# Optimization experiments

Hardware: AMD Instinct MI355X
Metric: run time of the kernel (lower is better)

## Reference

```python
import jax, jax.numpy as jnp
import numpy as np

# Multi-scale feature pyramid (H, W) per level, as produced by a DETR backbone
SPATIAL_SHAPES = [(100, 100), (50, 50), (25, 25), (13, 13)]
LEVEL_START = np.cumsum([0] + [h * w for h, w in SPATIAL_SHAPES])[:-1]
LEN = sum(h * w for h, w in SPATIAL_SHAPES)  # 13294
B = 2
D = 256      # d_model
NH = 8       # n_heads
NL = 4       # n_levels
NP = 4       # n_points
DH = D // NH
DFF = 1024
EPS = 1e-5


def setup_inputs() -> dict:
    key = jax.random.key(0)
    ks = jax.random.split(key, 16)
    w = lambda k, sh: jax.random.normal(k, sh, jnp.float32) * 0.02
    return {
        'src': jax.random.normal(ks[0], (B, LEN, D), jnp.float32),
        'pos': jax.random.normal(ks[1], (B, LEN, D), jnp.float32) * 0.02,
        'reference_points': jax.random.uniform(ks[2], (B, LEN, NL, 2), jnp.float32),
        'W_value': w(ks[3], (D, D)), 'b_value': jnp.zeros((D,), jnp.float32),
        'W_off': w(ks[4], (D, NH * NL * NP * 2)), 'b_off': w(ks[5], (NH * NL * NP * 2,)),
        'W_attn': w(ks[6], (D, NH * NL * NP)), 'b_attn': jnp.zeros((NH * NL * NP,), jnp.float32),
        'W_out': w(ks[7], (D, D)), 'b_out': jnp.zeros((D,), jnp.float32),
        'W1': w(ks[8], (D, DFF)), 'b1': jnp.zeros((DFF,), jnp.float32),
        'W2': w(ks[9], (DFF, D)), 'b2': jnp.zeros((D,), jnp.float32),
        'g1': jnp.ones((D,), jnp.float32), 'be1': jnp.zeros((D,), jnp.float32),
        'g2': jnp.ones((D,), jnp.float32), 'be2': jnp.zeros((D,), jnp.float32),
    }


def layer_norm(x, g, b):
    m = jnp.mean(x, -1, keepdims=True)
    v = jnp.mean((x - m) ** 2, -1, keepdims=True)
    return (x - m) * jax.lax.rsqrt(v + EPS) * g + b


def ms_deform_attn(query, src, ref, W_value, b_value, W_off, b_off, W_attn, b_attn, W_out, b_out):
    Bq, L, _ = query.shape
    value = (src @ W_value + b_value).reshape(Bq, L, NH, DH)
    off = (query @ W_off + b_off).reshape(Bq, L, NH, NL, NP, 2)
    attw = jax.nn.softmax((query @ W_attn + b_attn).reshape(Bq, L, NH, NL * NP), axis=-1)
    attw = attw.reshape(Bq, L, NH, NL, NP)
    # normalizer is (W, H) per level, matching offset_normalizer in MSDeformAttn
    wh = jnp.array([[w_, h_] for h_, w_ in SPATIAL_SHAPES], jnp.float32)
    loc = ref[:, :, None, :, None, :] + off / wh[None, None, None, :, None, :]  # (B,L,NH,NL,NP,2)

    out = jnp.zeros((Bq, L, NH, DH), value.dtype)
    for l, (H, W) in enumerate(SPATIAL_SHAPES):
        s = int(LEVEL_START[l])
        vl = value[:, s:s + H * W]  # (B, H*W, NH, DH)
        # grid_sample(align_corners=False): pixel = loc * size - 0.5
        x = loc[:, :, :, l, :, 0] * W - 0.5  # (B, L, NH, NP)
        y = loc[:, :, :, l, :, 1] * H - 0.5
        x = jnp.transpose(x, (0, 1, 3, 2)).reshape(Bq, L * NP, NH)
        y = jnp.transpose(y, (0, 1, 3, 2)).reshape(Bq, L * NP, NH)
        x0 = jnp.floor(x); y0 = jnp.floor(y)
        dx = x - x0; dy = y - y0
        x0i = x0.astype(jnp.int32); y0i = y0.astype(jnp.int32)
        acc = jnp.zeros((Bq, L * NP, NH, DH), value.dtype)
        corners = [
            (x0i,     y0i,     (1 - dx) * (1 - dy)),
            (x0i + 1, y0i,     dx * (1 - dy)),
            (x0i,     y0i + 1, (1 - dx) * dy),
            (x0i + 1, y0i + 1, dx * dy),
        ]
        for xi, yi, wgt in corners:
            inb = (xi >= 0) & (xi < W) & (yi >= 0) & (yi < H)  # zero padding
            idx = jnp.clip(yi, 0, H - 1) * W + jnp.clip(xi, 0, W - 1)
            g = jnp.take_along_axis(vl, idx[..., None], axis=1)  # (B, L*NP, NH, DH)
            acc = acc + g * (wgt * inb)[..., None]
        acc = acc.reshape(Bq, L, NP, NH, DH)
        w_l = jnp.transpose(attw[:, :, :, l, :], (0, 1, 3, 2))  # (B, L, NP, NH)
        out = out + jnp.sum(acc * w_l[..., None], axis=2)
    return out.reshape(Bq, L, D) @ W_out + b_out


def reference(src, pos, reference_points,
              W_value, b_value, W_off, b_off, W_attn, b_attn, W_out, b_out,
              W1, b1, W2, b2, g1, be1, g2, be2):
    # DeformableTransformerEncoderLayer.forward (dropout = identity at eval)
    query = src + pos
    src2 = ms_deform_attn(query, src, reference_points,
                          W_value, b_value, W_off, b_off, W_attn, b_attn, W_out, b_out)
    src = layer_norm(src + src2, g1, be1)
    ffn = jax.nn.relu(src @ W1 + b1) @ W2 + b2
    src = layer_norm(src + ffn, g2, be2)
    return src
```

## Files before the change

kernel.cpp:

```cpp
#include <hip/hip_runtime.h>
#include <hip/hip_bf16.h>

#define LENQ 13294
#define MROWS 26588
#define PADM  26624
#define EPS_LN 1e-5f

typedef __attribute__((ext_vector_type(8))) short short8;
typedef __attribute__((ext_vector_type(4))) float vf4;

__device__ inline ushort f2bf(float f) {
    __hip_bfloat16 h = __float2bfloat16(f);
    return reinterpret_cast<ushort&>(h);
}
__device__ inline float bfbits2f(uint lo16) {
    return __uint_as_float(lo16 << 16);
}

__device__ inline void load_lds16(const void* g, void* l) {
    __builtin_amdgcn_global_load_lds(
        (const __attribute__((address_space(1))) unsigned int*)g,
        (__attribute__((address_space(3))) unsigned int*)l,
        16, 0, 0);
}

__global__ __launch_bounds__(256) void wconv_all(
    const float* __restrict__ Wv, const float* __restrict__ Woff,
    const float* __restrict__ Wattn, const float* __restrict__ Wout,
    const float* __restrict__ W1, const float* __restrict__ W2,
    ushort* __restrict__ wvt, ushort* __restrict__ woat,
    ushort* __restrict__ woutt, ushort* __restrict__ w1t, ushort* __restrict__ w2t)
{
    const int bid = blockIdx.x;
    const float* src; ushort* dst; int K, N, tb;
    if      (bid < 64)  { src = Wv;    dst = wvt;            K = 256;  N = 256;  tb = bid; }
    else if (bid < 128) { src = Woff;  dst = woat;           K = 256;  N = 256;  tb = bid - 64; }
    else if (bid < 160) { src = Wattn; dst = woat + 256*256; K = 256;  N = 128;  tb = bid - 128; }
    else if (bid < 224) { src = Wout;  dst = woutt;          K = 256;  N = 256;  tb = bid - 160; }
    else if (bid < 480) { src = W1;    dst = w1t;            K = 256;  N = 1024; tb = bid - 224; }
    else                { src = W2;    dst = w2t;            K = 1024; N = 256;  tb = bid - 480; }
    const int ntn = N >> 5;
    const int kt = tb / ntn, nt = tb % ntn;

    __shared__ float s[32][36];
    const int t = threadIdx.x;
    const int ty = t >> 3, tx = (t & 7) * 4;
    float4 v = *reinterpret_cast<const float4*>(src + (size_t)(kt*32 + ty) * N + nt*32 + tx);
    s[ty][tx+0] = v.x; s[ty][tx+1] = v.y; s[ty][tx+2] = v.z; s[ty][tx+3] = v.w;
    __syncthreads();
    ushort4 o;
    o.x = f2bf(s[tx+0][ty]); o.y = f2bf(s[tx+1][ty]);
    o.z = f2bf(s[tx+2][ty]); o.w = f2bf(s[tx+3][ty]);
    *reinterpret_cast<ushort4*>(dst + (size_t)(nt*32 + ty) * K + kt*32 + tx) = o;
}

__global__ __launch_bounds__(256) void conv_src_q(
    const float* __restrict__ src, const float* __restrict__ pos,
    ushort* __restrict__ srcb, ushort* __restrict__ qb)
{
    const int i = blockIdx.x * 256 + threadIdx.x;
    const int row = i >> 6;
    const int c4 = i & 63;
    const int sr = min(row, MROWS - 1);
    float4 s = reinterpret_cast<const float4*>(src)[(size_t)sr * 64 + c4];
    float4 p = reinterpret_cast<const float4*>(pos)[(size_t)sr * 64 + c4];
    ushort4 sb, qv;
    sb.x = f2bf(s.x); sb.y = f2bf(s.y); sb.z = f2bf(s.z); sb.w = f2bf(s.w);
    qv.x = f2bf(s.x + p.x); qv.y = f2bf(s.y + p.y);
    qv.z = f2bf(s.z + p.z); qv.w = f2bf(s.w + p.w);
    reinterpret_cast<ushort4*>(srcb)[(size_t)row * 64 + c4] = sb;
    reinterpret_cast<ushort4*>(qb)[(size_t)row * 64 + c4]   = qv;
}

template<int MF, bool RELU>
__global__ __launch_bounds__(256) void gemm_lds(
    const ushort* __restrict__ A, const ushort* __restrict__ Bt,
    const float* __restrict__ bias0, const float* __restrict__ bias1, int nsplit,
    ushort* __restrict__ C, int N, int K)
{
    constexpr int BM = MF * 32;
    __shared__ short As[BM * 32];
    __shared__ short Bs[128 * 32];

    const int t = threadIdx.x;
    const int m0 = blockIdx.x * BM, n0 = blockIdx.y * 128;
    const int lane = t & 63, w = t >> 6;
    const int wr = w >> 1, wc = w & 1;
    const int ln = lane & 15, lr = lane >> 4;
    const int swz = (lr ^ ((ln >> 1) & 3)) * 8;
    const int cg = (((lane & 3) ^ ((lane >> 3) & 3))) * 8;
    const int srow = lane >> 2;

    vf4 acc[MF][4];
    #pragma unroll
    for (int m = 0; m < MF; ++m)
        #pragma unroll
        for (int n = 0; n < 4; ++n)
            acc[m][n] = (vf4){0.f, 0.f, 0.f, 0.f};

    const int bch0 = 2 * w, bch1 = 2 * w + 1;
    const ushort* gB0 = Bt + (size_t)(n0 + bch0 * 16 + srow) * K + cg;
    const ushort* gB1 = Bt + (size_t)(n0 + bch1 * 16 + srow) * K + cg;
    short* lB0 = Bs + bch0 * 512;
    short* lB1 = Bs + bch1 * 512;
    const int ach0 = (MF == 4) ? 2 * w : w;
    const ushort* gA0 = A + (size_t)(m0 + ach0 * 16 + srow) * K + cg;
    short* lA0 = As + ach0 * 512;
    const ushort* gA1 = A + (size_t)(m0 + (2 * w + 1) * 16 + srow) * K + cg;
    short* lA1 = As + (2 * w + 1) * 512;

    for (int k0 = 0; k0 < K; k0 += 32) {
        __syncthreads();
        load_lds16(gA0 + k0, lA0);
        if constexpr (MF == 4) load_lds16(gA1 + k0, lA1);
        load_lds16(gB0 + k0, lB0);
        load_lds16(gB1 + k0, lB1);
        __syncthreads();

        short8 af[MF], bfr[4];
        #pragma unroll
        for (int m = 0; m < MF; ++m)
            af[m] = *reinterpret_cast<const short8*>(&As[(wr * (MF * 16) + m * 16 + ln) * 32 + swz]);
        #pragma unroll
        for (int n = 0; n < 4; ++n)
            bfr[n] = *reinterpret_cast<const short8*>(&Bs[(wc * 64 + n * 16 + ln) * 32 + swz]);
        #pragma unroll
        for (int m = 0; m < MF; ++m)
            #pragma unroll
            for (int n = 0; n < 4; ++n)
                acc[m][n] = __builtin_amdgcn_mfma_f32_16x16x32_bf16(af[m], bfr[n], acc[m][n], 0, 0, 0);
    }

    #pragma unroll
    for (int n = 0; n < 4; ++n) {
        const int col = n0 + wc * 64 + n * 16 + ln;
        const float b = (col < nsplit) ? bias0[col] : bias1[col - nsplit];
        #pragma unroll
        for (int m = 0; m < MF; ++m) {
            const int rbase = m0 + wr * (MF * 16) + m * 16 + lr * 4;
            #pragma unroll
            for (int q = 0; q < 4; ++q) {
                float v = acc[m][n][q] + b;
                if (RELU) v = fmaxf(v, 0.f);
                C[(size_t)(rbase + q) * N + col] = f2bf(v);
            }
        }
    }
}

__global__ __launch_bounds__(256) void ms_sample(
    const ushort* __restrict__ value, const ushort* __restrict__ oa,
    const float* __restrict__ ref, ushort* __restrict__ outb)
{
    __shared__ uint2 s_iw[32 * 68];

    const int t    = threadIdx.x;
    const int row0 = blockIdx.x * 4;

    #pragma unroll
    for (int j = 0; j < 2; ++j) {
        const int item = t + j * 256;
        const int r = item >> 7, h = (item >> 4) & 7, lp = item & 15;
        const int l = lp >> 2;
        const int row = row0 + r;
        const int bsel = (row >= LENQ) ? 1 : 0;

        const float lg = bfbits2f(oa[(size_t)row * 384 + 256 + h * 16 + lp]);
        float mx = lg;
        #pragma unroll
        for (int s2 = 1; s2 < 16; s2 <<= 1) mx = fmaxf(mx, __shfl_xor(mx, s2));
        const float e = __expf(lg - mx);
        float se = e;
        #pragma unroll
        for (int s2 = 1; s2 < 16; s2 <<= 1) se += __shfl_xor(se, s2);
        const float aw = e / se;

        const int W = (int)((0x0D193264u >> (l * 8)) & 0xffu);
        const int LS = (l == 0) ? 0 : (l == 1) ? 10000 : (l == 2) ? 12500 : 13125;
        const uint oxy = *reinterpret_cast<const uint*>(oa + (size_t)row * 384 + (h * 16 + lp) * 2);
        const float ox = bfbits2f(oxy & 0xffffu);
        const float oy = __uint_as_float(oxy & 0xffff0000u);
        const float rx = ref[(size_t)row * 8 + l * 2 + 0];
        const float ry = ref[(size_t)row * 8 + l * 2 + 1];
        const float fw = (float)W;
        const float x = (rx + ox / fw) * fw - 0.5f;
        const float y = (ry + oy / fw) * fw - 0.5f;
        const float fx = floorf(x), fy = floorf(y);
        const float dx = x - fx, dy = y - fy;
        const int x0 = (int)fx, y0 = (int)fy;
        const int gbase = bsel * LENQ + LS;
        uint2* dst = &s_iw[(r * 8 + h) * 68 + lp * 4];
        #pragma unroll
        for (int cy = 0; cy < 2; ++cy)
            #pragma unroll
            for (int cx = 0; cx < 2; ++cx) {
                const int xi = x0 + cx, yi = y0 + cy;
                const bool in = (xi >= 0) && (xi < W) && (yi >= 0) && (yi < W);
                const int xc = min(max(xi, 0), W - 1);
                const int yc = min(max(yi, 0), W - 1);
                const float wgt = in ? ((cx ? dx : 1.f - dx) * (cy ? dy : 1.f - dy) * aw) : 0.f;
                dst[cy * 2 + cx] = make_uint2((uint)((gbase + yc * W + xc) * 256),
                                              __float_as_uint(wgt));
            }
    }
    __syncthreads();

    const int r = t >> 6, h = (t >> 3) & 7, c4 = t & 7;
    const int row = row0 + r;
    const ushort* vb = value + h * 32 + c4 * 4;
    const uint2* iw = &s_iw[(r * 8 + h) * 68];
    float4 acc = make_float4(0.f, 0.f, 0.f, 0.f);
    #pragma unroll 8
    for (int e = 0; e < 64; ++e) {
        const uint2 w = iw[e];
        const float wt = __uint_as_float(w.y);
        const uint2 gv = *reinterpret_cast<const uint2*>(vb + w.x);
        acc.x += wt * __uint_as_float(gv.x << 16);
        acc.y += wt * __uint_as_float(gv.x & 0xffff0000u);
        acc.z += wt * __uint_as_float(gv.y << 16);
        acc.w += wt * __uint_as_float(gv.y & 0xffff0000u);
    }
    ushort4 o;
    o.x = f2bf(acc.x); o.y = f2bf(acc.y); o.z = f2bf(acc.z); o.w = f2bf(acc.w);
    *reinterpret_cast<ushort4*>(outb + (size_t)row * 256 + h * 32 + c4 * 4) = o;
}

template<bool AF32, bool WF32>
__global__ __launch_bounds__(256) void resid_ln(
    const float* __restrict__ af, const ushort* __restrict__ ab,
    const ushort* __restrict__ r,
    const float* __restrict__ g, const float* __restrict__ be,
    float* __restrict__ outf, ushort* __restrict__ outb, int M)
{
    const int lane = threadIdx.x & 63;
    const int wid  = threadIdx.x >> 6;
    const int row  = blockIdx.x * 4 + wid;
    if (row >= M) return;

    float4 va;
    if (AF32) {
        va = *(reinterpret_cast<const float4*>(af + (size_t)row * 256) + lane);
    } else {
        ushort4 ua = *(reinterpret_cast<const ushort4*>(ab + (size_t)row * 256) + lane);
        va.x = bfbits2f(ua.x); va.y = bfbits2f(ua.y);
        va.z = bfbits2f(ua.z); va.w = bfbits2f(ua.w);
    }
    ushort4 ur = *(reinterpret_cast<const ushort4*>(r + (size_t)row * 256) + lane);
    float4 v;
    v.x = va.x + bfbits2f(ur.x); v.y = va.y + bfbits2f(ur.y);
    v.z = va.z + bfbits2f(ur.z); v.w = va.w + bfbits2f(ur.w);

    float s = v.x + v.y + v.z + v.w;
    #pragma unroll
    for (int m = 1; m < 64; m <<= 1) s += __shfl_xor(s, m);
    const float mean = s * (1.f / 256.f);

    float4 d;
    d.x = v.x - mean; d.y = v.y - mean; d.z = v.z - mean; d.w = v.w - mean;
    float q = d.x * d.x + d.y * d.y + d.z * d.z + d.w * d.w;
    #pragma unroll
    for (int m = 1; m < 64; m <<= 1) q += __shfl_xor(q, m);
    const float rs = rsqrtf(q * (1.f / 256.f) + EPS_LN);

    float4 gv = *(reinterpret_cast<const float4*>(g) + lane);
    float4 bv = *(reinterpret_cast<const float4*>(be) + lane);
    float4 o;
    o.x = d.x * rs * gv.x + bv.x;
    o.y = d.y * rs * gv.y + bv.y;
    o.z = d.z * rs * gv.z + bv.z;
    o.w = d.w * rs * gv.w + bv.w;
    if (WF32) {
        *(reinterpret_cast<float4*>(outf + (size_t)row * 256) + lane) = o;
    } else {
        ushort4 h;
        h.x = f2bf(o.x); h.y = f2bf(o.y); h.z = f2bf(o.z); h.w = f2bf(o.w);
        *(reinterpret_cast<ushort4*>(outb + (size_t)row * 256) + lane) = h;
    }
}

extern "C" void kernel_launch(void* const* d_in, const int* in_sizes, int n_in,
                              void* d_out, int out_size, void* d_ws, size_t ws_size,
                              hipStream_t stream)
{
    const float* src   = (const float*)d_in[0];
    const float* pos   = (const float*)d_in[1];
    const float* refp  = (const float*)d_in[2];
    const float* Wv    = (const float*)d_in[3];
    const float* bv    = (const float*)d_in[4];
    const float* Woff  = (const float*)d_in[5];
    const float* boff  = (const float*)d_in[6];
    const float* Wattn = (const float*)d_in[7];
    const float* battn = (const float*)d_in[8];
    const float* Wout  = (const float*)d_in[9];
    const float* bout  = (const float*)d_in[10];
    const float* W1    = (const float*)d_in[11];
    const float* b1    = (const float*)d_in[12];
    const float* W2    = (const float*)d_in[13];
    const float* b2    = (const float*)d_in[14];
    const float* g1    = (const float*)d_in[15];
    const float* be1   = (const float*)d_in[16];
    const float* g2    = (const float*)d_in[17];
    const float* be2   = (const float*)d_in[18];
    float* out = (float*)d_out;

    char* wsb = (char*)d_ws;
    const size_t SB   = (size_t)PADM * 256 * 2;
    const size_t OABS = (size_t)PADM * 384 * 2;
    ushort* srcb   = (ushort*)(wsb);
    ushort* qb     = (ushort*)(wsb + SB);
    ushort* valueb = (ushort*)(wsb + 2 * SB);
    ushort* oab    = (ushort*)(wsb + 3 * SB);
    ushort* attnb  = (ushort*)(wsb + 3 * SB + OABS);
    ushort* src2b  = (ushort*)(wsb + 4 * SB + OABS);
    ushort* ffnb   = src2b;
    ushort* x1b    = (ushort*)(wsb + 5 * SB + OABS);
    ushort* hb     = (ushort*)(wsb);
    char*   wgt    = wsb + 6 * SB + OABS;
    ushort* wvt    = (ushort*)(wgt);
    ushort* woat   = (ushort*)(wgt + 131072);
    ushort* woutt  = (ushort*)(wgt + 327680);
    ushort* w1t    = (ushort*)(wgt + 458752);
    ushort* w2t    = (ushort*)(wgt + 983040);

    const dim3 blk(256);

    wconv_all<<<dim3(736), blk, 0, stream>>>(Wv, Woff, Wattn, Wout, W1, W2,
                                             wvt, woat, woutt, w1t, w2t);

    conv_src_q<<<dim3(PADM / 4), blk, 0, stream>>>(src, pos, srcb, qb);

    gemm_lds<2, false><<<dim3(416, 2), blk, 0, stream>>>(
        srcb, wvt, bv, bv, 256, valueb, 256, 256);

    gemm_lds<2, false><<<dim3(416, 3), blk, 0, stream>>>(
        qb, woat, boff, battn, 256, oab, 384, 256);

    ms_sample<<<dim3(6647), blk, 0, stream>>>(valueb, oab, refp, attnb);

    gemm_lds<2, false><<<dim3(416, 2), blk, 0, stream>>>(
        attnb, woutt, bout, bout, 256, src2b, 256, 256);

    resid_ln<true, false><<<dim3(6647), blk, 0, stream>>>(
        src, nullptr, src2b, g1, be1, nullptr, x1b, MROWS);

    gemm_lds<4, true><<<dim3(208, 8), blk, 0, stream>>>(
        x1b, w1t, b1, b1, 1024, hb, 1024, 256);

    gemm_lds<2, false><<<dim3(416, 2), blk, 0, stream>>>(
        hb, w2t, b2, b2, 256, ffnb, 256, 1024);

    resid_ln<false, true><<<dim3(6647), blk, 0, stream>>>(
        nullptr, x1b, ffnb, g2, be2, out, nullptr, MROWS);
}
```

Measured before the change: 195.0 us.

## Double-buffer GEMM LDS tiles and widen deformable-sampling gathers to 16 bytes

The GEMM kernel now keeps two LDS buffers per operand. It prefetches the next K-tile while running MFMAs on the current one, which drops one of the two barriers per iteration. The ms_sample kernel now handles 8 query rows per block with 4 threads per head, each gathering 16-byte (8 bf16) value vectors. Corner indices and weights are packed as uint4 pairs, aiming to halve gather instruction count and raise per-thread memory parallelism. This costs double the LDS in the GEMM and larger sampling LDS, which may lower occupancy, and the async LDS loads may still be serialized by compiler waits.

After: 182.4 us. 1.07x faster.

```diff
diff --git a/kernel.cpp b/kernel.cpp
--- a/kernel.cpp
+++ b/kernel.cpp
@@ -16,6 +16,8 @@
 __device__ inline float bfbits2f(uint lo16) {
     return __uint_as_float(lo16 << 16);
 }
+__device__ inline float lo16f(uint u) { return __uint_as_float(u << 16); }
+__device__ inline float hi16f(uint u) { return __uint_as_float(u & 0xffff0000u); }
 
 __device__ inline void load_lds16(const void* g, void* l) {
     __builtin_amdgcn_global_load_lds(
@@ -79,8 +81,8 @@
     ushort* __restrict__ C, int N, int K)
 {
     constexpr int BM = MF * 32;
-    __shared__ short As[BM * 32];
-    __shared__ short Bs[128 * 32];
+    __shared__ short As[2][BM * 32];
+    __shared__ short Bs[2][128 * 32];
 
     const int t = threadIdx.x;
     const int m0 = blockIdx.x * BM, n0 = blockIdx.y * 128;
@@ -98,38 +100,44 @@
         for (int n = 0; n < 4; ++n)
             acc[m][n] = (vf4){0.f, 0.f, 0.f, 0.f};
 
-    const int bch0 = 2 * w, bch1 = 2 * w + 1;
-    const ushort* gB0 = Bt + (size_t)(n0 + bch0 * 16 + srow) * K + cg;
-    const ushort* gB1 = Bt + (size_t)(n0 + bch1 * 16 + srow) * K + cg;
-    short* lB0 = Bs + bch0 * 512;
-    short* lB1 = Bs + bch1 * 512;
     const int ach0 = (MF == 4) ? 2 * w : w;
     const ushort* gA0 = A + (size_t)(m0 + ach0 * 16 + srow) * K + cg;
-    short* lA0 = As + ach0 * 512;
     const ushort* gA1 = A + (size_t)(m0 + (2 * w + 1) * 16 + srow) * K + cg;
-    short* lA1 = As + (2 * w + 1) * 512;
-
+    const ushort* gB0 = Bt + (size_t)(n0 + (2 * w) * 16 + srow) * K + cg;
+    const ushort* gB1 = Bt + (size_t)(n0 + (2 * w + 1) * 16 + srow) * K + cg;
+    const int lA0 = ach0 * 512, lA1 = (2 * w + 1) * 512;
+    const int lB0 = (2 * w) * 512, lB1 = (2 * w + 1) * 512;
+
+#define STAGE_TILE(buf, kk) do {                                        \
+        load_lds16(gA0 + (kk), &As[buf][lA0]);                          \
+        if constexpr (MF == 4) load_lds16(gA1 + (kk), &As[buf][lA1]);   \
+        load_lds16(gB0 + (kk), &Bs[buf][lB0]);                          \
+        load_lds16(gB1 + (kk), &Bs[buf][lB1]);                          \
+    } while (0)
+
+    STAGE_TILE(0, 0);
+    int cur = 0;
     for (int k0 = 0; k0 < K; k0 += 32) {
         __syncthreads();
-        load_lds16(gA0 + k0, lA0);
-        if constexpr (MF == 4) load_lds16(gA1 + k0, lA1);
-        load_lds16(gB0 + k0, lB0);
-        load_lds16(gB1 + k0, lB1);
-        __syncthreads();
+        if (k0 + 32 < K) STAGE_TILE(cur ^ 1, k0 + 32);
 
         short8 af[MF], bfr[4];
         #pragma unroll
         for (int m = 0; m < MF; ++m)
-            af[m] = *reinterpret_cast<const short8*>(&As[(wr * (MF * 16) + m * 16 + ln) * 32 + swz]);
+            af[m] = *reinterpret_cast<const short8*>(
+                &As[cur][(wr * (MF * 16) + m * 16 + ln) * 32 + swz]);
         #pragma unroll
         for (int n = 0; n < 4; ++n)
-            bfr[n] = *reinterpret_cast<const short8*>(&Bs[(wc * 64 + n * 16 + ln) * 32 + swz]);
+            bfr[n] = *reinterpret_cast<const short8*>(
+                &Bs[cur][(wc * 64 + n * 16 + ln) * 32 + swz]);
         #pragma unroll
         for (int m = 0; m < MF; ++m)
             #pragma unroll
             for (int n = 0; n < 4; ++n)
                 acc[m][n] = __builtin_amdgcn_mfma_f32_16x16x32_bf16(af[m], bfr[n], acc[m][n], 0, 0, 0);
-    }
+        cur ^= 1;
+    }
+#undef STAGE_TILE
 
     #pragma unroll
     for (int n = 0; n < 4; ++n) {
@@ -152,17 +160,17 @@
     const ushort* __restrict__ value, const ushort* __restrict__ oa,
     const float* __restrict__ ref, ushort* __restrict__ outb)
 {
-    __shared__ uint2 s_iw[32 * 68];
+    __shared__ uint2 s_iw[64 * 66];
 
     const int t    = threadIdx.x;
-    const int row0 = blockIdx.x * 4;
-
-    #pragma unroll
-    for (int j = 0; j < 2; ++j) {
+    const int row0 = blockIdx.x * 8;
+
+    #pragma unroll
+    for (int j = 0; j < 4; ++j) {
         const int item = t + j * 256;
         const int r = item >> 7, h = (item >> 4) & 7, lp = item & 15;
         const int l = lp >> 2;
-        const int row = row0 + r;
+        const int row = min(row0 + r, MROWS - 1);
         const int bsel = (row >= LENQ) ? 1 : 0;
 
         const float lg = bfbits2f(oa[(size_t)row * 384 + 256 + h * 16 + lp]);
@@ -178,8 +186,8 @@
         const int W = (int)((0x0D193264u >> (l * 8)) & 0xffu);
         const int LS = (l == 0) ? 0 : (l == 1) ? 10000 : (l == 2) ? 12500 : 13125;
         const uint oxy = *reinterpret_cast<const uint*>(oa + (size_t)row * 384 + (h * 16 + lp) * 2);
-        const float ox = bfbits2f(oxy & 0xffffu);
-        const float oy = __uint_as_float(oxy & 0xffff0000u);
+        const float ox = lo16f(oxy);
+        const float oy = hi16f(oxy);
         const float rx = ref[(size_t)row * 8 + l * 2 + 0];
         const float ry = ref[(size_t)row * 8 + l * 2 + 1];
         const float fw = (float)W;
@@ -188,41 +196,64 @@
         const float fx = floorf(x), fy = floorf(y);
         const float dx = x - fx, dy = y - fy;
         const int x0 = (int)fx, y0 = (int)fy;
+        const int x1i = x0 + 1, y1i = y0 + 1;
         const int gbase = bsel * LENQ + LS;
-        uint2* dst = &s_iw[(r * 8 + h) * 68 + lp * 4];
-        #pragma unroll
-        for (int cy = 0; cy < 2; ++cy)
-            #pragma unroll
-            for (int cx = 0; cx < 2; ++cx) {
-                const int xi = x0 + cx, yi = y0 + cy;
-                const bool in = (xi >= 0) && (xi < W) && (yi >= 0) && (yi < W);
-                const int xc = min(max(xi, 0), W - 1);
-                const int yc = min(max(yi, 0), W - 1);
-                const float wgt = in ? ((cx ? dx : 1.f - dx) * (cy ? dy : 1.f - dy) * aw) : 0.f;
-                dst[cy * 2 + cx] = make_uint2((uint)((gbase + yc * W + xc) * 256),
-                                              __float_as_uint(wgt));
-            }
+
+        const bool inx0 = (x0 >= 0) && (x0 < W), inx1 = (x1i >= 0) && (x1i < W);
+        const bool iny0 = (y0 >= 0) && (y0 < W), iny1 = (y1i >= 0) && (y1i < W);
+        const int xc0 = min(max(x0, 0), W - 1), xc1 = min(max(x1i, 0), W - 1);
+        const int yc0 = min(max(y0, 0), W - 1), yc1 = min(max(y1i, 0), W - 1);
+        const float w00 = (inx0 && iny0) ? (1.f - dx) * (1.f - dy) * aw : 0.f;
+        const float w10 = (inx1 && iny0) ? dx * (1.f - dy) * aw : 0.f;
+        const float w01 = (inx0 && iny1) ? (1.f - dx) * dy * aw : 0.f;
+        const float w11 = (inx1 && iny1) ? dx * dy * aw : 0.f;
+        const uint b0 = (uint)(gbase + yc0 * W);
+        const uint b1 = (uint)(gbase + yc1 * W);
+        uint4 c01, c23;
+        c01.x = (b0 + (uint)xc0) * 512u; c01.y = __float_as_uint(w00);
+        c01.z = (b0 + (uint)xc1) * 512u; c01.w = __float_as_uint(w10);
+        c23.x = (b1 + (uint)xc0) * 512u; c23.y = __float_as_uint(w01);
+        c23.z = (b1 + (uint)xc1) * 512u; c23.w = __float_as_uint(w11);
+        uint4* dst = reinterpret_cast<uint4*>(&s_iw[(r * 8 + h) * 66 + lp * 4]);
+        dst[0] = c01;
+        dst[1] = c23;
     }
     __syncthreads();
 
-    const int r = t >> 6, h = (t >> 3) & 7, c4 = t & 7;
+    const int g = t >> 2, cq = t & 3;
+    const int r = g >> 3, h = g & 7;
+    const char* vbase = (const char*)value + h * 64 + cq * 16;
+    const uint4* iw = reinterpret_cast<const uint4*>(&s_iw[g * 66]);
+    float acc[8] = {0.f, 0.f, 0.f, 0.f, 0.f, 0.f, 0.f, 0.f};
+    #pragma unroll 4
+    for (int e2 = 0; e2 < 32; ++e2) {
+        const uint4 p = iw[e2];
+        {
+            const uint4 gv = *reinterpret_cast<const uint4*>(vbase + p.x);
+            const float w0 = __uint_as_float(p.y);
+            acc[0] += w0 * lo16f(gv.x); acc[1] += w0 * hi16f(gv.x);
+            acc[2] += w0 * lo16f(gv.y); acc[3] += w0 * hi16f(gv.y);
+            acc[4] += w0 * lo16f(gv.z); acc[5] += w0 * hi16f(gv.z);
+            acc[6] += w0 * lo16f(gv.w); acc[7] += w0 * hi16f(gv.w);
+        }
+        {
+            const uint4 gv = *reinterpret_cast<const uint4*>(vbase + p.z);
+            const float w1 = __uint_as_float(p.w);
+            acc[0] += w1 * lo16f(gv.x); acc[1] += w1 * hi16f(gv.x);
+            acc[2] += w1 * lo16f(gv.y); acc[3] += w1 * hi16f(gv.y);
+            acc[4] += w1 * lo16f(gv.z); acc[5] += w1 * hi16f(gv.z);
+            acc[6] += w1 * lo16f(gv.w); acc[7] += w1 * hi16f(gv.w);
+        }
+    }
     const int row = row0 + r;
-    const ushort* vb = value + h * 32 + c4 * 4;
-    const uint2* iw = &s_iw[(r * 8 + h) * 68];
-    float4 acc = make_float4(0.f, 0.f, 0.f, 0.f);
-    #pragma unroll 8
-    for (int e = 0; e < 64; ++e) {
-        const uint2 w = iw[e];
-        const float wt = __uint_as_float(w.y);
-        const uint2 gv = *reinterpret_cast<const uint2*>(vb + w.x);
-        acc.x += wt * __uint_as_float(gv.x << 16);
-        acc.y += wt * __uint_as_float(gv.x & 0xffff0000u);
-        acc.z += wt * __uint_as_float(gv.y << 16);
-        acc.w += wt * __uint_as_float(gv.y & 0xffff0000u);
-    }
-    ushort4 o;
-    o.x = f2bf(acc.x); o.y = f2bf(acc.y); o.z = f2bf(acc.z); o.w = f2bf(acc.w);
-    *reinterpret_cast<ushort4*>(outb + (size_t)row * 256 + h * 32 + c4 * 4) = o;
+    if (row < MROWS) {
+        uint4 o;
+        o.x = (uint)f2bf(acc[0]) | ((uint)f2bf(acc[1]) << 16);
+        o.y = (uint)f2bf(acc[2]) | ((uint)f2bf(acc[3]) << 16);
+        o.z = (uint)f2bf(acc[4]) | ((uint)f2bf(acc[5]) << 16);
+        o.w = (uint)f2bf(acc[6]) | ((uint)f2bf(acc[7]) << 16);
+        *reinterpret_cast<uint4*>((char*)outb + (size_t)row * 512 + h * 64 + cq * 16) = o;
+    }
 }
 
 template<bool AF32, bool WF32>
@@ -335,7 +366,7 @@
     gemm_lds<2, false><<<dim3(416, 3), blk, 0, stream>>>(
         qb, woat, boff, battn, 256, oab, 384, 256);
 
-    ms_sample<<<dim3(6647), blk, 0, stream>>>(valueb, oab, refp, attnb);
+    ms_sample<<<dim3(3324), blk, 0, stream>>>(valueb, oab, refp, attnb);
 
     gemm_lds<2, false><<<dim3(416, 2), blk, 0, stream>>>(
         attnb, woutt, bout, bout, 256, src2b, 256, 256);
```
